# Performance work log

Measured on AMD Instinct MI355X. Metric: run time of the kernel, lower is better.

## Reference

```python
import jax, jax.numpy as jnp
import numpy as np

B, N, C = 4, 2048, 1024
H = 8
D = C // H  # head dim = 128
SCALE = D ** -0.5
EPS = 1e-5


def setup_inputs() -> dict:
    key = jax.random.key(0)
    ks = jax.random.split(key, 12)
    s = 0.02
    return {
        "x": jax.random.normal(ks[0], (B, N, C), jnp.float32),
        "ln1_g": jnp.ones((C,), jnp.float32),
        "ln1_b": jnp.zeros((C,), jnp.float32),
        "w_qkv": jax.random.normal(ks[1], (3 * C, C), jnp.float32) * s,  # torch Linear weight [out,in], no bias
        "w_proj": jax.random.normal(ks[2], (C, C), jnp.float32) * s,
        "b_proj": jnp.zeros((C,), jnp.float32),
        "ln2_g": jnp.ones((C,), jnp.float32),
        "ln2_b": jnp.zeros((C,), jnp.float32),
        "w1": jax.random.normal(ks[3], (C, C), jnp.float32) * s,
        "b1": jnp.full((C,), 0.1, jnp.float32),
        "w2": jax.random.normal(ks[4], (C, C), jnp.float32) * s,
        "b2": jnp.full((C,), 0.1, jnp.float32),
        "bn_g": jnp.ones((C,), jnp.float32),
        "bn_b": jnp.zeros((C,), jnp.float32),
        "bn_mean": jnp.zeros((C,), jnp.float32),
        "bn_var": jnp.ones((C,), jnp.float32),
    }


def _layernorm(x, g, b):
    mu = jnp.mean(x, axis=-1, keepdims=True)
    var = jnp.mean(jnp.square(x - mu), axis=-1, keepdims=True)
    return (x - mu) * jax.lax.rsqrt(var + EPS) * g + b


def reference(x, ln1_g, ln1_b, w_qkv, w_proj, b_proj, ln2_g, ln2_b,
              w1, b1, w2, b2, bn_g, bn_b, bn_mean, bn_var):
    # --- attention branch (pre-LN) ---
    h = _layernorm(x, ln1_g, ln1_b)
    qkv = h @ w_qkv.T                              # [B,N,3C]
    qkv = qkv.reshape(B, N, 3, H, D)
    q = qkv[:, :, 0].transpose(0, 2, 1, 3)         # [B,H,N,D]
    k = qkv[:, :, 1].transpose(0, 2, 1, 3)
    v = qkv[:, :, 2].transpose(0, 2, 1, 3)
    attn = jnp.einsum('bhnd,bhmd->bhnm', q, k) * SCALE
    attn = jax.nn.softmax(attn, axis=-1)
    o = jnp.einsum('bhnm,bhmd->bhnd', attn, v)     # [B,H,N,D]
    o = o.transpose(0, 2, 1, 3).reshape(B, N, C)
    x = x + (o @ w_proj.T + b_proj)

    # --- MLP branch (pre-LN), ELU + eval-mode BatchNorm ---
    h = _layernorm(x, ln2_g, ln2_b)
    h = jax.nn.elu(h @ w1.T + b1)
    h = jax.nn.elu(h @ w2.T + b2)
    h = (h - bn_mean) * jax.lax.rsqrt(bn_var + EPS) * bn_g + bn_b
    return x + h
```

## Files before the change

kernel.cpp:

```cpp
#include <hip/hip_runtime.h>
#include <hip/hip_bf16.h>

using u16 = unsigned short;
typedef __attribute__((ext_vector_type(8))) __bf16 bf16x8;
typedef __attribute__((ext_vector_type(4))) float f32x4;
typedef __attribute__((ext_vector_type(16))) float f32x16;
typedef __attribute__((ext_vector_type(4))) unsigned int u32x4;

#define LN_EPS 1e-5f
#define ATT_SCALE 0.08838834764831845f

__device__ __forceinline__ u16 f2bf(float f) {
    unsigned int u = __builtin_bit_cast(unsigned int, f);
    u += 0x7FFFu + ((u >> 16) & 1u);
    return (u16)(u >> 16);
}

__device__ __forceinline__ bf16x8 ld_frag(const u16* p) {
    return __builtin_bit_cast(bf16x8, *(const u32x4*)p);
}

__device__ __forceinline__ unsigned pack_bf2(float lo, float hi) {
    return __builtin_amdgcn_perm(__builtin_bit_cast(unsigned, hi),
                                 __builtin_bit_cast(unsigned, lo), 0x07060302u);
}

__device__ __forceinline__ void gl_lds(const u16* g, u16* l) {
    __builtin_amdgcn_global_load_lds((const __attribute__((address_space(1))) void*)g,
                                     (__attribute__((address_space(3))) void*)l, 16, 0, 0);
}

__global__ void cvt_f32_bf16(const float* __restrict__ in, u16* __restrict__ out, int n4) {
    int i = blockIdx.x * blockDim.x + threadIdx.x;
    if (i < n4) {
        const float4 v = ((const float4*)in)[i];
        ushort4 o;
        o.x = f2bf(v.x); o.y = f2bf(v.y); o.z = f2bf(v.z); o.w = f2bf(v.w);
        ((ushort4*)out)[i] = o;
    }
}

__global__ __launch_bounds__(256)
void ln_kernel(const float* __restrict__ x, const float* __restrict__ g,
               const float* __restrict__ b, u16* __restrict__ out)
{
    const int row = blockIdx.x;
    const int t = threadIdx.x;
    const float4 v = ((const float4*)(x + (size_t)row * 1024))[t];
    float s  = v.x + v.y + v.z + v.w;
    float ss = v.x * v.x + v.y * v.y + v.z * v.z + v.w * v.w;
    #pragma unroll
    for (int d = 32; d > 0; d >>= 1) { s += __shfl_down(s, d); ss += __shfl_down(ss, d); }
    __shared__ float red[8];
    const int wave = t >> 6, lane = t & 63;
    if (lane == 0) { red[wave] = s; red[4 + wave] = ss; }
    __syncthreads();
    const float S  = red[0] + red[1] + red[2] + red[3];
    const float SS = red[4] + red[5] + red[6] + red[7];
    const float mu = S * (1.f / 1024.f);
    const float rstd = rsqrtf(SS * (1.f / 1024.f) - mu * mu + LN_EPS);
    const float4 gv = ((const float4*)g)[t];
    const float4 bv = ((const float4*)b)[t];
    ushort4 ov;
    ov.x = f2bf((v.x - mu) * rstd * gv.x + bv.x);
    ov.y = f2bf((v.y - mu) * rstd * gv.y + bv.y);
    ov.z = f2bf((v.z - mu) * rstd * gv.z + bv.z);
    ov.w = f2bf((v.w - mu) * rstd * gv.w + bv.w);
    ((ushort4*)(out + (size_t)row * 1024))[t] = ov;
}

__global__ __launch_bounds__(256, 2)
void gemm_qkv(const u16* __restrict__ A, const u16* __restrict__ Bw,
              u16* __restrict__ Cb, u16* __restrict__ Cv)
{
    const int M = 8192, N = 3072, K = 1024;
    __shared__ __align__(16) u16 As[128 * 32];
    __shared__ __align__(16) u16 Bs[128 * 32];

    const int tid  = threadIdx.x;
    const int wave = tid >> 6;
    const int lane = tid & 63;
    const int quad = lane >> 4;
    const int l16  = lane & 15;
    const int m0 = blockIdx.x * 128;
    const int n0 = blockIdx.y * 128;
    const int wm = (wave & 1) * 64;
    const int wn = (wave >> 1) * 64;

    f32x4 acc[4][4];
    #pragma unroll
    for (int i = 0; i < 4; i++)
        #pragma unroll
        for (int j = 0; j < 4; j++)
            acc[i][j] = f32x4{0.f, 0.f, 0.f, 0.f};

    const int srow = lane >> 2;
    const int scol = (lane & 3) * 8;
    const u16* gA0 = A  + (size_t)(m0 + wave * 32 + srow) * K + scol;
    const u16* gA1 = gA0 + (size_t)16 * K;
    const u16* gB0 = Bw + (size_t)(n0 + wave * 32 + srow) * K + scol;
    const u16* gB1 = gB0 + (size_t)16 * K;
    u16* lA0 = &As[(wave * 32) * 32];
    u16* lA1 = &As[(wave * 32 + 16) * 32];
    u16* lB0 = &Bs[(wave * 32) * 32];
    u16* lB1 = &Bs[(wave * 32 + 16) * 32];

    for (int k0 = 0; k0 < K; k0 += 32) {
        gl_lds(gA0 + k0, lA0);
        gl_lds(gA1 + k0, lA1);
        gl_lds(gB0 + k0, lB0);
        gl_lds(gB1 + k0, lB1);
        __syncthreads();
        bf16x8 af[4], bfv[4];
        #pragma unroll
        for (int i = 0; i < 4; i++) af[i]  = ld_frag(&As[(wm + i * 16 + l16) * 32 + quad * 8]);
        #pragma unroll
        for (int j = 0; j < 4; j++) bfv[j] = ld_frag(&Bs[(wn + j * 16 + l16) * 32 + quad * 8]);
        #pragma unroll
        for (int i = 0; i < 4; i++)
            #pragma unroll
            for (int j = 0; j < 4; j++)
                acc[i][j] = __builtin_amdgcn_mfma_f32_16x16x32_bf16(af[i], bfv[j], acc[i][j], 0, 0, 0);
        __syncthreads();
    }

    #pragma unroll
    for (int j = 0; j < 4; j++) {
        const int gn = n0 + wn + j * 16 + l16;
        if (gn < 2048) {
            const float qs = (gn < 1024) ? ATT_SCALE : 1.0f;
            #pragma unroll
            for (int i = 0; i < 4; i++) {
                const int gm0 = m0 + wm + i * 16 + quad * 4;
                #pragma unroll
                for (int r = 0; r < 4; r++)
                    Cb[(size_t)(gm0 + r) * 2048 + gn] = f2bf(acc[i][j][r] * qs);
            }
        } else {
            const int hh = (gn >> 7) & 7, dd = gn & 127;
            #pragma unroll
            for (int i = 0; i < 4; i++) {
                const int gm0 = m0 + wm + i * 16 + quad * 4;
                #pragma unroll
                for (int r = 0; r < 4; r++) {
                    const int tok = gm0 + r;
                    Cv[((size_t)((tok >> 11) * 8 + hh) * 128 + dd) * 2048 + (tok & 2047)] =
                        f2bf(acc[i][j][r]);
                }
            }
        }
    }
}

template <int EPI>
__global__ __launch_bounds__(256, 4)
void gemm_c(const u16* __restrict__ A, const u16* __restrict__ Bw,
            const float* __restrict__ bias, const float* __restrict__ res,
            float* __restrict__ Cf, u16* __restrict__ Cb,
            const float* __restrict__ bng, const float* __restrict__ bnb,
            const float* __restrict__ bnm, const float* __restrict__ bnv)
{
    const int N = 1024, K = 1024;
    __shared__ __align__(16) u16 As[64 * 32];
    __shared__ __align__(16) u16 Bs[128 * 32];

    const int tid  = threadIdx.x;
    const int wave = tid >> 6;
    const int lane = tid & 63;
    const int quad = lane >> 4;
    const int l16  = lane & 15;
    const int m0 = blockIdx.x * 64;
    const int n0 = blockIdx.y * 128;
    const int wm = (wave & 1) * 32;
    const int wn = (wave >> 1) * 64;

    f32x4 acc[2][4];
    #pragma unroll
    for (int i = 0; i < 2; i++)
        #pragma unroll
        for (int j = 0; j < 4; j++)
            acc[i][j] = f32x4{0.f, 0.f, 0.f, 0.f};

    const int srow = tid >> 2;
    const int scol = (tid & 3) * 8;
    const u16* gA  = A  + (size_t)(m0 + srow) * K + scol;
    const u16* gB0 = Bw + (size_t)(n0 + srow) * K + scol;
    const u16* gB1 = gB0 + (size_t)64 * K;
    u16* lA  = &As[wave * 512];
    u16* lB0 = &Bs[wave * 512];
    u16* lB1 = &Bs[2048 + wave * 512];

    for (int k0 = 0; k0 < K; k0 += 32) {
        gl_lds(gA  + k0, lA);
        gl_lds(gB0 + k0, lB0);
        gl_lds(gB1 + k0, lB1);
        __syncthreads();
        bf16x8 af[2], bfv[4];
        #pragma unroll
        for (int i = 0; i < 2; i++) af[i]  = ld_frag(&As[(wm + i * 16 + l16) * 32 + quad * 8]);
        #pragma unroll
        for (int j = 0; j < 4; j++) bfv[j] = ld_frag(&Bs[(wn + j * 16 + l16) * 32 + quad * 8]);
        #pragma unroll
        for (int i = 0; i < 2; i++)
            #pragma unroll
            for (int j = 0; j < 4; j++)
                acc[i][j] = __builtin_amdgcn_mfma_f32_16x16x32_bf16(af[i], bfv[j], acc[i][j], 0, 0, 0);
        __syncthreads();
    }

    #pragma unroll
    for (int j = 0; j < 4; j++) {
        const int gn = n0 + wn + j * 16 + l16;
        float bs = bias[gn], sc = 0.f, sh = 0.f;
        if constexpr (EPI == 3) {
            const float iv = rsqrtf(bnv[gn] + LN_EPS);
            sc = bng[gn] * iv;
            sh = bnb[gn] - bnm[gn] * sc;
        }
        #pragma unroll
        for (int i = 0; i < 2; i++) {
            const int gm0 = m0 + wm + i * 16 + quad * 4;
            #pragma unroll
            for (int r = 0; r < 4; r++) {
                const size_t idx = (size_t)(gm0 + r) * N + gn;
                const float v = acc[i][j][r];
                if constexpr (EPI == 1) {
                    Cf[idx] = res[idx] + v + bs;
                } else if constexpr (EPI == 2) {
                    float t = v + bs;
                    t = t > 0.f ? t : (__expf(t) - 1.f);
                    Cb[idx] = f2bf(t);
                } else {
                    float t = v + bs;
                    t = t > 0.f ? t : (__expf(t) - 1.f);
                    t = t * sc + sh;
                    Cf[idx] = res[idx] + t;
                }
            }
        }
    }
}

__global__ __launch_bounds__(256, 2)
void attn_kernel(const u16* __restrict__ qk, const u16* __restrict__ vT, u16* __restrict__ o)
{
    __shared__ __align__(16) u16 smem[32768];

    const int tid  = threadIdx.x;
    const int wave = tid >> 6;
    const int lane = tid & 63;
    const int l32  = lane & 31;
    const int hl   = lane >> 5;
    const int id   = blockIdx.x;
    const int bh   = ((id >> 7) << 3) | (id & 7);
    const int qt   = (id >> 3) & 15;
    const int b    = bh >> 3, h = bh & 7;
    const size_t tok0 = (size_t)b * 2048;

    const u16* qptr = qk + h * 128;
    const u16* kptr = qk + 1024 + h * 128;
    const u16* vptr = vT + (size_t)bh * 128 * 2048;

    #pragma unroll
    for (int qq = 0; qq < 8; qq++) {
        const int s = qq * 256 + tid;
        const int r = s >> 4;
        const int cg = (s & 15) ^ (r & 7);
        const u16* g = qptr + (tok0 + qt * 128 + r) * 2048 + cg * 8;
        const int sb = 16384 + (qq * 256 + (tid & 192)) * 8;
        gl_lds(g, smem + sb);
    }
    __syncthreads();

    bf16x8 qf[8];
    {
        const int row = wave * 32 + l32;
        #pragma unroll
        for (int ks = 0; ks < 8; ks++) {
            const int c = (ks * 2 + hl) ^ (row & 7);
            qf[ks] = ld_frag(smem + 16384 + row * 128 + c * 8);
        }
    }

    f32x16 oacc[4];
    #pragma unroll
    for (int i = 0; i < 4; i++)
        #pragma unroll
        for (int e = 0; e < 16; e++) oacc[i][e] = 0.f;
    float l_acc = 0.f;

    {
        #pragma unroll
        for (int qq = 0; qq < 4; qq++) {
            const int s = qq * 256 + tid;
            const int rk = s >> 4, ck = (s & 15) ^ (rk & 7);
            gl_lds(kptr + (tok0 + rk) * 2048 + ck * 8,
                   smem + (qq * 256 + (tid & 192)) * 8);
            const int rv = s >> 3, cv = (s & 7) ^ (rv & 7);
            gl_lds(vptr + (size_t)rv * 2048 + cv * 8,
                   smem + 8192 + (qq * 256 + (tid & 192)) * 8);
        }
    }

    for (int kt = 0; kt < 32; kt++) {
        __syncthreads();

        if (kt + 1 < 32) {
            u16* nb = smem + ((kt + 1) & 1) * 16384;
            #pragma unroll
            for (int qq = 0; qq < 4; qq++) {
                const int s = qq * 256 + tid;
                const int rk = s >> 4, ck = (s & 15) ^ (rk & 7);
                gl_lds(kptr + (tok0 + (kt + 1) * 64 + rk) * 2048 + ck * 8,
                       nb + (qq * 256 + (tid & 192)) * 8);
                const int rv = s >> 3, cv = (s & 7) ^ (rv & 7);
                gl_lds(vptr + (size_t)rv * 2048 + (kt + 1) * 64 + cv * 8,
                       nb + 8192 + (qq * 256 + (tid & 192)) * 8);
            }
        }

        const u16* Ks = smem + (kt & 1) * 16384;
        const u16* Vs = Ks + 8192;

        f32x16 sacc[2];
        #pragma unroll
        for (int t = 0; t < 2; t++)
            #pragma unroll
            for (int e = 0; e < 16; e++) sacc[t][e] = 0.f;
        #pragma unroll
        for (int ks = 0; ks < 8; ks++) {
            #pragma unroll
            for (int mt = 0; mt < 2; mt++) {
                const int row = mt * 32 + l32;
                const int c = (ks * 2 + hl) ^ (row & 7);
                const bf16x8 kf = ld_frag(Ks + row * 128 + c * 8);
                sacc[mt] = __builtin_amdgcn_mfma_f32_32x32x16_bf16(kf, qf[ks], sacc[mt], 0, 0, 0);
            }
        }

        unsigned pk[2][8];
        #pragma unroll
        for (int t = 0; t < 2; t++) {
            #pragma unroll
            for (int r2 = 0; r2 < 8; r2++) {
                const float p0 = __expf(sacc[t][2 * r2]);
                const float p1 = __expf(sacc[t][2 * r2 + 1]);
                l_acc += p0 + p1;
                pk[t][r2] = pack_bf2(p0, p1);
            }
        }

        #pragma unroll
        for (int ks = 0; ks < 4; ks++) {
            const int t = ks >> 1;
            const int pb = (ks & 1) * 4;
            const unsigned s0 = (unsigned)__shfl_xor((int)pk[t][pb + 0], 32);
            const unsigned s1 = (unsigned)__shfl_xor((int)pk[t][pb + 1], 32);
            const unsigned s2 = (unsigned)__shfl_xor((int)pk[t][pb + 2], 32);
            const unsigned s3 = (unsigned)__shfl_xor((int)pk[t][pb + 3], 32);
            u32x4 pu;
            pu.x = hl ? s2 : pk[t][pb + 0];
            pu.y = hl ? s3 : pk[t][pb + 1];
            pu.z = hl ? pk[t][pb + 2] : s0;
            pu.w = hl ? pk[t][pb + 3] : s1;
            const bf16x8 pf = __builtin_bit_cast(bf16x8, pu);
            #pragma unroll
            for (int dt = 0; dt < 4; dt++) {
                const int row = dt * 32 + l32;
                const int c = (ks * 2 + hl) ^ (row & 7);
                const bf16x8 vf = ld_frag(Vs + row * 64 + c * 8);
                oacc[dt] = __builtin_amdgcn_mfma_f32_32x32x16_bf16(vf, pf, oacc[dt], 0, 0, 0);
            }
        }
    }

    __syncthreads();
    u16* Ot = smem;
    const float lt  = l_acc + __shfl_xor(l_acc, 32);
    const float inv = 1.0f / lt;
    const int qloc = wave * 32 + l32;
    #pragma unroll
    for (int dt = 0; dt < 4; dt++) {
        #pragma unroll
        for (int r2 = 0; r2 < 8; r2++) {
            const float v0 = oacc[dt][2 * r2] * inv;
            const float v1 = oacc[dt][2 * r2 + 1] * inv;
            const int dp = dt * 32 + 4 * hl + 2 * (r2 & 1) + 8 * (r2 >> 1);
            *(unsigned*)(Ot + qloc * 136 + dp) = pack_bf2(v0, v1);
        }
    }
    __syncthreads();
    const int qr = tid >> 1;
    const int hh = tid & 1;
    const u16* src = Ot + qr * 136 + hh * 64;
    u16* dst = o + (tok0 + qt * 128 + qr) * 1024 + h * 128 + hh * 64;
    #pragma unroll
    for (int c = 0; c < 8; c++)
        *(u32x4*)(dst + c * 8) = *(const u32x4*)(src + c * 8);
}

extern "C" void kernel_launch(void* const* d_in, const int* in_sizes, int n_in,
                              void* d_out, int out_size, void* d_ws, size_t ws_size,
                              hipStream_t stream)
{
    const float* x      = (const float*)d_in[0];
    const float* ln1_g  = (const float*)d_in[1];
    const float* ln1_b  = (const float*)d_in[2];
    const float* w_qkv  = (const float*)d_in[3];
    const float* w_proj = (const float*)d_in[4];
    const float* b_proj = (const float*)d_in[5];
    const float* ln2_g  = (const float*)d_in[6];
    const float* ln2_b  = (const float*)d_in[7];
    const float* w1     = (const float*)d_in[8];
    const float* b1     = (const float*)d_in[9];
    const float* w2     = (const float*)d_in[10];
    const float* b2     = (const float*)d_in[11];
    const float* bn_g   = (const float*)d_in[12];
    const float* bn_b   = (const float*)d_in[13];
    const float* bn_m   = (const float*)d_in[14];
    const float* bn_v   = (const float*)d_in[15];
    float* out = (float*)d_out;

    u16* wq   = (u16*)d_ws;
    u16* wp   = wq  + (size_t)3072 * 1024;
    u16* w1b  = wp  + (size_t)1024 * 1024;
    u16* w2b  = w1b + (size_t)1024 * 1024;
    u16* hbuf = w2b + (size_t)1024 * 1024;
    u16* qkb  = hbuf + (size_t)8192 * 1024;
    u16* vTb  = qkb + (size_t)8192 * 2048;
    u16* obuf = vTb + (size_t)8192 * 1024;
    float* x1 = (float*)(obuf + (size_t)8192 * 1024);

    cvt_f32_bf16<<<3072, 256, 0, stream>>>(w_qkv,  wq,  3072 * 1024 / 4);
    cvt_f32_bf16<<<1024, 256, 0, stream>>>(w_proj, wp,  1024 * 1024 / 4);
    cvt_f32_bf16<<<1024, 256, 0, stream>>>(w1,     w1b, 1024 * 1024 / 4);
    cvt_f32_bf16<<<1024, 256, 0, stream>>>(w2,     w2b, 1024 * 1024 / 4);

    ln_kernel<<<8192, 256, 0, stream>>>(x, ln1_g, ln1_b, hbuf);

    gemm_qkv<<<dim3(64, 24), 256, 0, stream>>>(hbuf, wq, qkb, vTb);

    attn_kernel<<<512, 256, 0, stream>>>(qkb, vTb, obuf);

    gemm_c<1><<<dim3(128, 8), 256, 0, stream>>>(obuf, wp,
        b_proj, x, x1, nullptr, nullptr, nullptr, nullptr, nullptr);

    ln_kernel<<<8192, 256, 0, stream>>>(x1, ln2_g, ln2_b, hbuf);

    gemm_c<2><<<dim3(128, 8), 256, 0, stream>>>(hbuf, w1b,
        b1, nullptr, nullptr, obuf, nullptr, nullptr, nullptr, nullptr);

    gemm_c<3><<<dim3(128, 8), 256, 0, stream>>>(obuf, w2b,
        b2, x1, out, nullptr, bn_g, bn_b, bn_m, bn_v);
}
```

Measured before the change: 400.4 us.

## Enlarge GEMM tiles to 128x128 and give each attention wave two query sub-tiles

The three C-sized GEMMs move from 64x128 to 128x128 block tiles, so each wave computes a 64x64 sub-tile and every B fragment is reused across twice as many rows. The attention kernel now handles 256 queries per block, with each wave holding two 32-query Q fragment sets, so each K/V fragment loaded from LDS feeds two MFMAs. Both changes cut global and LDS traffic per FLOP but raise register pressure (launch bounds lowered) and halve the grid: 256 attention blocks and 512 blocks per GEMM, which may underfill the 256 CUs and worsen tail effects. The output staging stride changes to 138 and the write-out is done in two passes.

```diff
diff --git a/kernel.cpp b/kernel.cpp
--- a/kernel.cpp
+++ b/kernel.cpp
@@ -73,7 +73,7 @@
 void gemm_qkv(const u16* __restrict__ A, const u16* __restrict__ Bw,
               u16* __restrict__ Cb, u16* __restrict__ Cv)
 {
-    const int M = 8192, N = 3072, K = 1024;
+    const int K = 1024;
     __shared__ __align__(16) u16 As[128 * 32];
     __shared__ __align__(16) u16 Bs[128 * 32];
 
@@ -153,7 +153,7 @@
 }
 
 template <int EPI>
-__global__ __launch_bounds__(256, 4)
+__global__ __launch_bounds__(256, 2)
 void gemm_c(const u16* __restrict__ A, const u16* __restrict__ Bw,
             const float* __restrict__ bias, const float* __restrict__ res,
             float* __restrict__ Cf, u16* __restrict__ Cb,
@@ -161,7 +161,7 @@
             const float* __restrict__ bnm, const float* __restrict__ bnv)
 {
     const int N = 1024, K = 1024;
-    __shared__ __align__(16) u16 As[64 * 32];
+    __shared__ __align__(16) u16 As[128 * 32];
     __shared__ __align__(16) u16 Bs[128 * 32];
 
     const int tid  = threadIdx.x;
@@ -169,39 +169,42 @@
     const int lane = tid & 63;
     const int quad = lane >> 4;
     const int l16  = lane & 15;
-    const int m0 = blockIdx.x * 64;
+    const int m0 = blockIdx.x * 128;
     const int n0 = blockIdx.y * 128;
-    const int wm = (wave & 1) * 32;
+    const int wm = (wave & 1) * 64;
     const int wn = (wave >> 1) * 64;
 
-    f32x4 acc[2][4];
-    #pragma unroll
-    for (int i = 0; i < 2; i++)
+    f32x4 acc[4][4];
+    #pragma unroll
+    for (int i = 0; i < 4; i++)
         #pragma unroll
         for (int j = 0; j < 4; j++)
             acc[i][j] = f32x4{0.f, 0.f, 0.f, 0.f};
 
-    const int srow = tid >> 2;
-    const int scol = (tid & 3) * 8;
-    const u16* gA  = A  + (size_t)(m0 + srow) * K + scol;
-    const u16* gB0 = Bw + (size_t)(n0 + srow) * K + scol;
-    const u16* gB1 = gB0 + (size_t)64 * K;
-    u16* lA  = &As[wave * 512];
-    u16* lB0 = &Bs[wave * 512];
-    u16* lB1 = &Bs[2048 + wave * 512];
+    const int srow = lane >> 2;
+    const int scol = (lane & 3) * 8;
+    const u16* gA0 = A  + (size_t)(m0 + wave * 32 + srow) * K + scol;
+    const u16* gA1 = gA0 + (size_t)16 * K;
+    const u16* gB0 = Bw + (size_t)(n0 + wave * 32 + srow) * K + scol;
+    const u16* gB1 = gB0 + (size_t)16 * K;
+    u16* lA0 = &As[(wave * 32) * 32];
+    u16* lA1 = &As[(wave * 32 + 16) * 32];
+    u16* lB0 = &Bs[(wave * 32) * 32];
+    u16* lB1 = &Bs[(wave * 32 + 16) * 32];
 
     for (int k0 = 0; k0 < K; k0 += 32) {
-        gl_lds(gA  + k0, lA);
+        gl_lds(gA0 + k0, lA0);
+        gl_lds(gA1 + k0, lA1);
         gl_lds(gB0 + k0, lB0);
         gl_lds(gB1 + k0, lB1);
         __syncthreads();
-        bf16x8 af[2], bfv[4];
-        #pragma unroll
-        for (int i = 0; i < 2; i++) af[i]  = ld_frag(&As[(wm + i * 16 + l16) * 32 + quad * 8]);
+        bf16x8 af[4], bfv[4];
+        #pragma unroll
+        for (int i = 0; i < 4; i++) af[i]  = ld_frag(&As[(wm + i * 16 + l16) * 32 + quad * 8]);
         #pragma unroll
         for (int j = 0; j < 4; j++) bfv[j] = ld_frag(&Bs[(wn + j * 16 + l16) * 32 + quad * 8]);
         #pragma unroll
-        for (int i = 0; i < 2; i++)
+        for (int i = 0; i < 4; i++)
             #pragma unroll
             for (int j = 0; j < 4; j++)
                 acc[i][j] = __builtin_amdgcn_mfma_f32_16x16x32_bf16(af[i], bfv[j], acc[i][j], 0, 0, 0);
@@ -218,7 +221,7 @@
             sh = bnb[gn] - bnm[gn] * sc;
         }
         #pragma unroll
-        for (int i = 0; i < 2; i++) {
+        for (int i = 0; i < 4; i++) {
             const int gm0 = m0 + wm + i * 16 + quad * 4;
             #pragma unroll
             for (int r = 0; r < 4; r++) {
@@ -241,7 +244,7 @@
     }
 }
 
-__global__ __launch_bounds__(256, 2)
+__global__ __launch_bounds__(256, 1)
 void attn_kernel(const u16* __restrict__ qk, const u16* __restrict__ vT, u16* __restrict__ o)
 {
     __shared__ __align__(16) u16 smem[32768];
@@ -252,54 +255,56 @@
     const int l32  = lane & 31;
     const int hl   = lane >> 5;
     const int id   = blockIdx.x;
-    const int bh   = ((id >> 7) << 3) | (id & 7);
-    const int qt   = (id >> 3) & 15;
+    const int bh   = id & 31;
+    const int qt   = id >> 5;
     const int b    = bh >> 3, h = bh & 7;
     const size_t tok0 = (size_t)b * 2048;
+    const int q0   = qt * 256;
 
     const u16* qptr = qk + h * 128;
     const u16* kptr = qk + 1024 + h * 128;
     const u16* vptr = vT + (size_t)bh * 128 * 2048;
 
     #pragma unroll
-    for (int qq = 0; qq < 8; qq++) {
+    for (int qq = 0; qq < 16; qq++) {
         const int s = qq * 256 + tid;
         const int r = s >> 4;
         const int cg = (s & 15) ^ (r & 7);
-        const u16* g = qptr + (tok0 + qt * 128 + r) * 2048 + cg * 8;
-        const int sb = 16384 + (qq * 256 + (tid & 192)) * 8;
-        gl_lds(g, smem + sb);
+        gl_lds(qptr + (tok0 + q0 + r) * 2048 + cg * 8,
+               smem + (qq * 256 + (tid & 192)) * 8);
     }
     __syncthreads();
 
-    bf16x8 qf[8];
-    {
-        const int row = wave * 32 + l32;
+    bf16x8 qf[2][8];
+    #pragma unroll
+    for (int h2 = 0; h2 < 2; h2++) {
+        const int row = wave * 64 + h2 * 32 + l32;
         #pragma unroll
         for (int ks = 0; ks < 8; ks++) {
             const int c = (ks * 2 + hl) ^ (row & 7);
-            qf[ks] = ld_frag(smem + 16384 + row * 128 + c * 8);
-        }
-    }
-
-    f32x16 oacc[4];
+            qf[h2][ks] = ld_frag(smem + row * 128 + c * 8);
+        }
+    }
+    __syncthreads();
+
+    f32x16 oacc[4][2];
     #pragma unroll
     for (int i = 0; i < 4; i++)
         #pragma unroll
-        for (int e = 0; e < 16; e++) oacc[i][e] = 0.f;
-    float l_acc = 0.f;
-
-    {
-        #pragma unroll
-        for (int qq = 0; qq < 4; qq++) {
-            const int s = qq * 256 + tid;
-            const int rk = s >> 4, ck = (s & 15) ^ (rk & 7);
-            gl_lds(kptr + (tok0 + rk) * 2048 + ck * 8,
-                   smem + (qq * 256 + (tid & 192)) * 8);
-            const int rv = s >> 3, cv = (s & 7) ^ (rv & 7);
-            gl_lds(vptr + (size_t)rv * 2048 + cv * 8,
-                   smem + 8192 + (qq * 256 + (tid & 192)) * 8);
-        }
+        for (int h2 = 0; h2 < 2; h2++)
+            #pragma unroll
+            for (int e = 0; e < 16; e++) oacc[i][h2][e] = 0.f;
+    float l_acc[2] = {0.f, 0.f};
+
+    #pragma unroll
+    for (int qq = 0; qq < 4; qq++) {
+        const int s = qq * 256 + tid;
+        const int rk = s >> 4, ck = (s & 15) ^ (rk & 7);
+        gl_lds(kptr + (tok0 + rk) * 2048 + ck * 8,
+               smem + (qq * 256 + (tid & 192)) * 8);
+        const int rv = s >> 3, cv = (s & 7) ^ (rv & 7);
+        gl_lds(vptr + (size_t)rv * 2048 + cv * 8,
+               smem + 8192 + (qq * 256 + (tid & 192)) * 8);
     }
 
     for (int kt = 0; kt < 32; kt++) {
@@ -322,11 +327,13 @@
         const u16* Ks = smem + (kt & 1) * 16384;
         const u16* Vs = Ks + 8192;
 
-        f32x16 sacc[2];
-        #pragma unroll
-        for (int t = 0; t < 2; t++)
-            #pragma unroll
-            for (int e = 0; e < 16; e++) sacc[t][e] = 0.f;
+        f32x16 sacc[2][2];
+        #pragma unroll
+        for (int mt = 0; mt < 2; mt++)
+            #pragma unroll
+            for (int h2 = 0; h2 < 2; h2++)
+                #pragma unroll
+                for (int e = 0; e < 16; e++) sacc[mt][h2][e] = 0.f;
         #pragma unroll
         for (int ks = 0; ks < 8; ks++) {
             #pragma unroll
@@ -334,19 +341,23 @@
                 const int row = mt * 32 + l32;
                 const int c = (ks * 2 + hl) ^ (row & 7);
                 const bf16x8 kf = ld_frag(Ks + row * 128 + c * 8);
-                sacc[mt] = __builtin_amdgcn_mfma_f32_32x32x16_bf16(kf, qf[ks], sacc[mt], 0, 0, 0);
-            }
-        }
-
-        unsigned pk[2][8];
-        #pragma unroll
-        for (int t = 0; t < 2; t++) {
-            #pragma unroll
-            for (int r2 = 0; r2 < 8; r2++) {
-                const float p0 = __expf(sacc[t][2 * r2]);
-                const float p1 = __expf(sacc[t][2 * r2 + 1]);
-                l_acc += p0 + p1;
-                pk[t][r2] = pack_bf2(p0, p1);
+                sacc[mt][0] = __builtin_amdgcn_mfma_f32_32x32x16_bf16(kf, qf[0][ks], sacc[mt][0], 0, 0, 0);
+                sacc[mt][1] = __builtin_amdgcn_mfma_f32_32x32x16_bf16(kf, qf[1][ks], sacc[mt][1], 0, 0, 0);
+            }
+        }
+
+        unsigned pk[2][2][8];
+        #pragma unroll
+        for (int mt = 0; mt < 2; mt++) {
+            #pragma unroll
+            for (int h2 = 0; h2 < 2; h2++) {
+                #pragma unroll
+                for (int r2 = 0; r2 < 8; r2++) {
+                    const float p0 = __expf(sacc[mt][h2][2 * r2]);
+                    const float p1 = __expf(sacc[mt][h2][2 * r2 + 1]);
+                    l_acc[h2] += p0 + p1;
+                    pk[mt][h2][r2] = pack_bf2(p0, p1);
+                }
             }
         }
 
@@ -354,49 +365,62 @@
         for (int ks = 0; ks < 4; ks++) {
             const int t = ks >> 1;
             const int pb = (ks & 1) * 4;
-            const unsigned s0 = (unsigned)__shfl_xor((int)pk[t][pb + 0], 32);
-            const unsigned s1 = (unsigned)__shfl_xor((int)pk[t][pb + 1], 32);
-            const unsigned s2 = (unsigned)__shfl_xor((int)pk[t][pb + 2], 32);
-            const unsigned s3 = (unsigned)__shfl_xor((int)pk[t][pb + 3], 32);
-            u32x4 pu;
-            pu.x = hl ? s2 : pk[t][pb + 0];
-            pu.y = hl ? s3 : pk[t][pb + 1];
-            pu.z = hl ? pk[t][pb + 2] : s0;
-            pu.w = hl ? pk[t][pb + 3] : s1;
-            const bf16x8 pf = __builtin_bit_cast(bf16x8, pu);
+            bf16x8 pf[2];
+            #pragma unroll
+            for (int h2 = 0; h2 < 2; h2++) {
+                const unsigned s0 = (unsigned)__shfl_xor((int)pk[t][h2][pb + 0], 32);
+                const unsigned s1 = (unsigned)__shfl_xor((int)pk[t][h2][pb + 1], 32);
+                const unsigned s2 = (unsigned)__shfl_xor((int)pk[t][h2][pb + 2], 32);
+                const unsigned s3 = (unsigned)__shfl_xor((int)pk[t][h2][pb + 3], 32);
+                u32x4 pu;
+                pu.x = hl ? s2 : pk[t][h2][pb + 0];
+                pu.y = hl ? s3 : pk[t][h2][pb + 1];
+                pu.z = hl ? pk[t][h2][pb + 2] : s0;
+                pu.w = hl ? pk[t][h2][pb + 3] : s1;
+                pf[h2] = __builtin_bit_cast(bf16x8, pu);
+            }
             #pragma unroll
             for (int dt = 0; dt < 4; dt++) {
                 const int row = dt * 32 + l32;
                 const int c = (ks * 2 + hl) ^ (row & 7);
                 const bf16x8 vf = ld_frag(Vs + row * 64 + c * 8);
-                oacc[dt] = __builtin_amdgcn_mfma_f32_32x32x16_bf16(vf, pf, oacc[dt], 0, 0, 0);
+                oacc[dt][0] = __builtin_amdgcn_mfma_f32_32x32x16_bf16(vf, pf[0], oacc[dt][0], 0, 0, 0);
+                oacc[dt][1] = __builtin_amdgcn_mfma_f32_32x32x16_bf16(vf, pf[1], oacc[dt][1], 0, 0, 0);
             }
         }
     }
 
     __syncthreads();
     u16* Ot = smem;
-    const float lt  = l_acc + __shfl_xor(l_acc, 32);
-    const float inv = 1.0f / lt;
-    const int qloc = wave * 32 + l32;
-    #pragma unroll
-    for (int dt = 0; dt < 4; dt++) {
-        #pragma unroll
-        for (int r2 = 0; r2 < 8; r2++) {
-            const float v0 = oacc[dt][2 * r2] * inv;
-            const float v1 = oacc[dt][2 * r2 + 1] * inv;
-            const int dp = dt * 32 + 4 * hl + 2 * (r2 & 1) + 8 * (r2 >> 1);
-            *(unsigned*)(Ot + qloc * 136 + dp) = pack_bf2(v0, v1);
-        }
-    }
-    __syncthreads();
-    const int qr = tid >> 1;
-    const int hh = tid & 1;
-    const u16* src = Ot + qr * 136 + hh * 64;
-    u16* dst = o + (tok0 + qt * 128 + qr) * 1024 + h * 128 + hh * 64;
-    #pragma unroll
-    for (int c = 0; c < 8; c++)
-        *(u32x4*)(dst + c * 8) = *(const u32x4*)(src + c * 8);
+    float inv[2];
+    #pragma unroll
+    for (int h2 = 0; h2 < 2; h2++) {
+        const float lt = l_acc[h2] + __shfl_xor(l_acc[h2], 32);
+        inv[h2] = 1.0f / lt;
+    }
+    #pragma unroll
+    for (int p = 0; p < 2; p++) {
+        if (p) __syncthreads();
+        #pragma unroll
+        for (int dt = 0; dt < 4; dt++) {
+            #pragma unroll
+            for (int r2 = 0; r2 < 8; r2++) {
+                const float v0 = oacc[dt][p][2 * r2] * inv[p];
+                const float v1 = oacc[dt][p][2 * r2 + 1] * inv[p];
+                const int dp = dt * 32 + 4 * hl + 2 * (r2 & 1) + 8 * (r2 >> 1);
+                *(unsigned*)(Ot + (wave * 32 + l32) * 138 + dp) = pack_bf2(v0, v1);
+            }
+        }
+        __syncthreads();
+        const int qr = tid >> 1;
+        const int hh = tid & 1;
+        const u16* src = Ot + qr * 138 + hh * 64;
+        const size_t tok = tok0 + q0 + (qr >> 5) * 64 + p * 32 + (qr & 31);
+        u16* dst = o + tok * 1024 + h * 128 + hh * 64;
+        #pragma unroll
+        for (int c = 0; c < 8; c++)
+            *(u32x4*)(dst + c * 8) = *(const u32x4*)(src + c * 8);
+    }
 }
 
 extern "C" void kernel_launch(void* const* d_in, const int* in_sizes, int n_in,
@@ -440,16 +464,16 @@
 
     gemm_qkv<<<dim3(64, 24), 256, 0, stream>>>(hbuf, wq, qkb, vTb);
 
-    attn_kernel<<<512, 256, 0, stream>>>(qkb, vTb, obuf);
-
-    gemm_c<1><<<dim3(128, 8), 256, 0, stream>>>(obuf, wp,
+    attn_kernel<<<256, 256, 0, stream>>>(qkb, vTb, obuf);
+
+    gemm_c<1><<<dim3(64, 8), 256, 0, stream>>>(obuf, wp,
         b_proj, x, x1, nullptr, nullptr, nullptr, nullptr, nullptr);
 
     ln_kernel<<<8192, 256, 0, stream>>>(x1, ln2_g, ln2_b, hbuf);
 
-    gemm_c<2><<<dim3(128, 8), 256, 0, stream>>>(hbuf, w1b,
+    gemm_c<2><<<dim3(64, 8), 256, 0, stream>>>(hbuf, w1b,
         b1, nullptr, nullptr, obuf, nullptr, nullptr, nullptr, nullptr);
 
-    gemm_c<3><<<dim3(128, 8), 256, 0, stream>>>(obuf, w2b,
+    gemm_c<3><<<dim3(64, 8), 256, 0, stream>>>(obuf, w2b,
         b2, x1, out, nullptr, bn_g, bn_b, bn_m, bn_v);
 }
```

Measured after the change: 409.8 us. 2.3% more time.
